# Optimization experiments

Measured on AMD Instinct MI355X. Metric: run time of the kernel, lower is better.

The kernel has to match this reference:

```python
import jax, jax.numpy as jnp
import numpy as np

NUM_HEADS = 16
EPS = 1e-8


def _dyn_quant(x):
    # per-token symmetric int8 quantization (dynamic input scale)
    s = jnp.maximum(jnp.max(jnp.abs(x), axis=-1, keepdims=True) / 127.0, EPS)
    q = jnp.clip(jnp.round(x / s), -127.0, 127.0)
    return q, s


def _quant_weight(w):
    # per-output-channel symmetric int8 weight quantization; w: [out, in]
    s = jnp.maximum(jnp.max(jnp.abs(w), axis=1, keepdims=True) / 127.0, EPS)
    q = jnp.clip(jnp.round(w / s), -127.0, 127.0)
    return q, s


def _w8a8_linear(x, w, b):
    # W8A8 GEMM with int32-exact accumulation (values fit exactly in fp32),
    # dequantized by per-token input scale * per-channel weight scale.
    qx, sx = _dyn_quant(x)          # [B,N,C], [B,N,1]
    qw, sw = _quant_weight(w)       # [O,C],   [O,1]
    y = jnp.einsum('bnc,oc->bno', qx, qw) * (sx * sw[:, 0])
    return y + b


def setup_inputs() -> dict:
    key = jax.random.key(0)
    ks = jax.random.split(key, 9)
    B, N, L, C = 2, 4096, 512, 2048
    sc = 0.02  # realistic weight init scale
    return {
        'x':    jax.random.normal(ks[0], (B, N, C), jnp.float32),
        'cond': jax.random.normal(ks[1], (B, L, C), jnp.float32),
        'mask': jnp.zeros((B, N, L), jnp.float32),  # additive attention mask
        'wq': jax.random.normal(ks[2], (C, C), jnp.float32) * sc,
        'bq': jnp.zeros((C,), jnp.float32),
        'wk': jax.random.normal(ks[3], (C, C), jnp.float32) * sc,
        'bk': jnp.zeros((C,), jnp.float32),
        'wv': jax.random.normal(ks[4], (C, C), jnp.float32) * sc,
        'bv': jnp.zeros((C,), jnp.float32),
        'wo': jax.random.normal(ks[5], (C, C), jnp.float32) * sc,
        'bo': jnp.zeros((C,), jnp.float32),
    }


def reference(x, cond, mask, wq, bq, wk, bk, wv, bv, wo, bo):
    B, N, C = x.shape
    L = cond.shape[1]
    H = NUM_HEADS
    D = C // H
    inv_sqrt_d = np.float32(1.0 / np.sqrt(D))

    # quantized Q projection, fp K/V projections
    q = _w8a8_linear(x, wq, bq).reshape(B, N, H, D).transpose(0, 2, 1, 3)      # [B,H,N,D]
    k = (cond @ wk.T + bk).reshape(B, L, H, D).transpose(0, 2, 1, 3)           # [B,H,L,D]
    v = (cond @ wv.T + bv).reshape(B, L, H, D).transpose(0, 2, 1, 3)           # [B,H,L,D]

    # SDPA cross-attention with additive mask broadcast over heads
    scores = jnp.einsum('bhnd,bhld->bhnl', q, k) * inv_sqrt_d + mask[:, None]
    attn = jax.nn.softmax(scores, axis=-1)
    o = jnp.einsum('bhnl,bhld->bhnd', attn, v)
    o = o.transpose(0, 2, 1, 3).reshape(B, N, C)

    # fused quant_sum (per-token requant) + quantized output projection
    return _w8a8_linear(o, wo, bo)
```

## Files before the change

kernel.cpp:

```cpp
#include <hip/hip_runtime.h>
#include <cstdint>
#include <cstddef>


typedef __bf16 bf16;
typedef __bf16 bf16x8 __attribute__((ext_vector_type(8)));
typedef __bf16 bf16x4 __attribute__((ext_vector_type(4)));
typedef float  f32x4  __attribute__((ext_vector_type(4)));
typedef int    i32x4  __attribute__((ext_vector_type(4)));

#define DEV __device__ __forceinline__

static constexpr int CB = 2;
static constexpr int CN = 4096;
static constexpr int CL = 512;
static constexpr int CC = 2048;
static constexpr int CH = 16;
static constexpr int CD = 128;
static constexpr int TOK = CB * CN;
static constexpr int LR  = CB * CL;

DEV void gl_lds16(const void* g, void* l) {
  __builtin_amdgcn_global_load_lds(
      (const __attribute__((address_space(1))) unsigned int*)g,
      (__attribute__((address_space(3))) unsigned int*)l, 16, 0, 0);
}

DEV f32x4 mfma16(bf16x8 a, bf16x8 b, f32x4 c) {
  return __builtin_amdgcn_mfma_f32_16x16x32_bf16(a, b, c, 0, 0, 0);
}

DEV i32x4 mfma_i8(i32x4 a, i32x4 b, i32x4 c) {
  return __builtin_amdgcn_mfma_i32_16x16x64_i8(a, b, c, 0, 0, 0);
}

__global__ __launch_bounds__(256) void quant_rows_i8(
    const float* __restrict__ in, signed char* __restrict__ q,
    float* __restrict__ scale)
{
  const int r = blockIdx.x, t = threadIdx.x;
  const float* x = in + (size_t)r * CC;
  const float4 v0 = ((const float4*)x)[2 * t];
  const float4 v1 = ((const float4*)x)[2 * t + 1];
  float m = fmaxf(fmaxf(fmaxf(fabsf(v0.x), fabsf(v0.y)), fmaxf(fabsf(v0.z), fabsf(v0.w))),
                  fmaxf(fmaxf(fabsf(v1.x), fabsf(v1.y)), fmaxf(fabsf(v1.z), fabsf(v1.w))));
#pragma unroll
  for (int off = 32; off > 0; off >>= 1) m = fmaxf(m, __shfl_xor(m, off));
  __shared__ float sm[4];
  if ((t & 63) == 0) sm[t >> 6] = m;
  __syncthreads();
  m = fmaxf(fmaxf(sm[0], sm[1]), fmaxf(sm[2], sm[3]));
  const float s = fmaxf(m / 127.0f, 1e-8f);
  if (t == 0) scale[r] = s;
  const float a[8] = {v0.x, v0.y, v0.z, v0.w, v1.x, v1.y, v1.z, v1.w};
  int2 pk;
  int lo = 0, hi = 0;
#pragma unroll
  for (int j = 0; j < 4; j++) {
    const int b0 = (int)fminf(fmaxf(rintf(a[j]     / s), -127.f), 127.f);
    const int b1 = (int)fminf(fmaxf(rintf(a[4 + j] / s), -127.f), 127.f);
    lo |= (b0 & 255) << (8 * j);
    hi |= (b1 & 255) << (8 * j);
  }
  pk.x = lo; pk.y = hi;
  const int c0 = t * 8;
  const int f = (r >> 1) & 3;
  const int pos = (c0 & ~63) | ((((c0 >> 4) & 3) ^ f) << 4) | (c0 & 15);
  *(int2*)&q[(size_t)r * CC + pos] = pk;
}

__global__ __launch_bounds__(256) void split_pair_k(
    const float* __restrict__ in, bf16* __restrict__ hi, bf16* __restrict__ lo)
{
  const size_t i = (size_t)blockIdx.x * 256 + threadIdx.x;
  const float4 v = ((const float4*)in)[i];
  const float a[4] = {v.x, v.y, v.z, v.w};
  bf16x4 h4, l4;
#pragma unroll
  for (int j = 0; j < 4; j++) {
    bf16 h = (bf16)a[j];
    h4[j] = h;
    l4[j] = (bf16)(a[j] - (float)h);
  }
  ((bf16x4*)hi)[i] = h4;
  ((bf16x4*)lo)[i] = l4;
}

__global__ __launch_bounds__(256) void bias_split_k(
    const float* __restrict__ in, const float* __restrict__ bias,
    bf16* __restrict__ hi, bf16* __restrict__ lo)
{
  const size_t i = (size_t)blockIdx.x * 256 + threadIdx.x;
  const float4 v = ((const float4*)in)[i];
  const float4 bb = ((const float4*)bias)[i & (CC / 4 - 1)];
  const float a[4] = {v.x + bb.x, v.y + bb.y, v.z + bb.z, v.w + bb.w};
  bf16x4 h4, l4;
#pragma unroll
  for (int j = 0; j < 4; j++) {
    bf16 h = (bf16)a[j];
    h4[j] = h;
    l4[j] = (bf16)(a[j] - (float)h);
  }
  ((bf16x4*)hi)[i] = h4;
  ((bf16x4*)lo)[i] = l4;
}

__global__ __launch_bounds__(256) void bias_split_vt_k(
    const float* __restrict__ Vf, const float* __restrict__ bias,
    bf16* __restrict__ vth, bf16* __restrict__ vtl)
{
  __shared__ float tile[32][33];
  const int t = threadIdx.x;
  const int l0 = blockIdx.x * 32, d0 = blockIdx.y * 32, bh = blockIdx.z;
  const int b = bh >> 4, h = bh & 15;
  const int r = t >> 3, c4 = (t & 7) * 4;
  const float4 v = *(const float4*)&Vf[((size_t)b * CL + l0 + r) * CC + h * CD + d0 + c4];
  const float4 bb = *(const float4*)&bias[h * CD + d0 + c4];
  tile[r][c4 + 0] = v.x + bb.x;
  tile[r][c4 + 1] = v.y + bb.y;
  tile[r][c4 + 2] = v.z + bb.z;
  tile[r][c4 + 3] = v.w + bb.w;
  __syncthreads();
  bf16x4 h4, l4;
#pragma unroll
  for (int j = 0; j < 4; j++) {
    const float a = tile[c4 + j][r];
    const bf16 hh = (bf16)a;
    h4[j] = hh;
    l4[j] = (bf16)(a - (float)hh);
  }
  const size_t o = ((size_t)bh * CD + d0 + r) * CL + l0 + c4;
  *(bf16x4*)&vth[o] = h4;
  *(bf16x4*)&vtl[o] = l4;
}

template <int MODE>
__global__ __launch_bounds__(256) void gemm_i8(
    const signed char* __restrict__ A, const signed char* __restrict__ B,
    float* __restrict__ out0, bf16* __restrict__ outH, bf16* __restrict__ outL,
    const float* __restrict__ rowS, const float* __restrict__ colS,
    const float* __restrict__ bias, const int Nd, const int K)
{
  __shared__ signed char sA[2][128 * 64] __attribute__((aligned(16)));
  __shared__ signed char sB[2][128 * 64] __attribute__((aligned(16)));
  const int t = threadIdx.x;
  const int m0 = blockIdx.y * 128, n0 = blockIdx.x * 128;
  const int srow = t >> 2, scol = (t & 3) * 16;
  const signed char* aP = A + (size_t)(m0 + srow) * K + scol;
  const signed char* bP = B + (size_t)(n0 + srow) * K + scol;
  const int lane = t & 63, wave = t >> 6;
  const int wm = (wave >> 1) * 64, wn = (wave & 1) * 64;
  const int quad = lane >> 4, l16 = lane & 15;
  i32x4 acc[4][4] = {};

  gl_lds16(aP,                  &sA[0][t * 16]);
  gl_lds16(aP + (size_t)64 * K, &sA[0][4096 + t * 16]);
  gl_lds16(bP,                  &sB[0][t * 16]);
  gl_lds16(bP + (size_t)64 * K, &sB[0][4096 + t * 16]);
  __syncthreads();

  int cur = 0;
  for (int kb = 0; kb < K; kb += 64) {
    const int nx = kb + 64;
    if (nx < K) {
      gl_lds16(aP + nx,                  &sA[cur ^ 1][t * 16]);
      gl_lds16(aP + nx + (size_t)64 * K, &sA[cur ^ 1][4096 + t * 16]);
      gl_lds16(bP + nx,                  &sB[cur ^ 1][t * 16]);
      gl_lds16(bP + nx + (size_t)64 * K, &sB[cur ^ 1][4096 + t * 16]);
    }
    i32x4 fa[4], fb[4];
#pragma unroll
    for (int i = 0; i < 4; i++) {
      const int ra = wm + i * 16 + l16;
      const int rb = wn + i * 16 + l16;
      fa[i] = *(const i32x4*)&sA[cur][ra * 64 + (quad ^ ((ra >> 1) & 3)) * 16];
      fb[i] = *(const i32x4*)&sB[cur][rb * 64 + (quad ^ ((rb >> 1) & 3)) * 16];
    }
#pragma unroll
    for (int mt = 0; mt < 4; mt++)
#pragma unroll
      for (int nt = 0; nt < 4; nt++)
        acc[mt][nt] = mfma_i8(fa[mt], fb[nt], acc[mt][nt]);
    __syncthreads();
    cur ^= 1;
  }

#pragma unroll
  for (int mt = 0; mt < 4; mt++)
#pragma unroll
    for (int nt = 0; nt < 4; nt++)
#pragma unroll
      for (int rg = 0; rg < 4; rg++) {
        const int mr = m0 + wm + mt * 16 + quad * 4 + rg;
        const int nc = n0 + wn + nt * 16 + l16;
        const float a = (float)acc[mt][nt][rg];
        const float sc = rowS[mr] * colS[nc];
        const float v = a * sc + bias[nc];
        if (MODE == 0) {
          out0[(size_t)mr * Nd + nc] = v;
        } else {
          const bf16 h = (bf16)v;
          outH[(size_t)mr * Nd + nc] = h;
          outL[(size_t)mr * Nd + nc] = (bf16)(v - (float)h);
        }
      }
}

__global__ __launch_bounds__(256) void gemm_kv(
    const bf16* __restrict__ Ah, const bf16* __restrict__ Al,
    const bf16* __restrict__ B0h, const bf16* __restrict__ B0l,
    const bf16* __restrict__ B1h, const bf16* __restrict__ B1l,
    float* __restrict__ out0, float* __restrict__ out1,
    const int Nd, const int K, const int kLen)
{
  __shared__ bf16 sAh[128 * 32] __attribute__((aligned(16)));
  __shared__ bf16 sBh[128 * 32] __attribute__((aligned(16)));
  __shared__ bf16 sAl[128 * 32] __attribute__((aligned(16)));
  __shared__ bf16 sBl[128 * 32] __attribute__((aligned(16)));
  const int t = threadIdx.x;
  const int kv = blockIdx.z >> 2, chunk = blockIdx.z & 3;
  const bf16* Bh = kv ? B1h : B0h;
  const bf16* Bl = kv ? B1l : B0l;
  float* outF = kv ? out1 : out0;
  const int m0 = blockIdx.y * 128, n0 = blockIdx.x * 128;
  const int k0 = chunk * kLen;
  const int srow = t >> 2, scol = (t & 3) * 8;
  const bf16* aP  = Ah + (size_t)(m0 + srow) * K + k0 + scol;
  const bf16* bP  = Bh + (size_t)(n0 + srow) * K + k0 + scol;
  const bf16* aPl = Al + (size_t)(m0 + srow) * K + k0 + scol;
  const bf16* bPl = Bl + (size_t)(n0 + srow) * K + k0 + scol;
  const int lane = t & 63, wave = t >> 6;
  const int wm = (wave >> 1) * 64, wn = (wave & 1) * 64;
  const int quad = lane >> 4, l16 = lane & 15;
  f32x4 acc[4][4] = {};

  for (int kb = 0; kb < kLen; kb += 32) {
    __syncthreads();
    gl_lds16(aP + kb,                   &sAh[t * 8]);
    gl_lds16(aP + kb + (size_t)64 * K,  &sAh[2048 + t * 8]);
    gl_lds16(bP + kb,                   &sBh[t * 8]);
    gl_lds16(bP + kb + (size_t)64 * K,  &sBh[2048 + t * 8]);
    gl_lds16(aPl + kb,                  &sAl[t * 8]);
    gl_lds16(aPl + kb + (size_t)64 * K, &sAl[2048 + t * 8]);
    gl_lds16(bPl + kb,                  &sBl[t * 8]);
    gl_lds16(bPl + kb + (size_t)64 * K, &sBl[2048 + t * 8]);
    __syncthreads();
    bf16x8 fa[4], fb[4], fal[4], fbl[4];
#pragma unroll
    for (int i = 0; i < 4; i++) {
      fa[i]  = *(const bf16x8*)&sAh[(wm + i * 16 + l16) * 32 + quad * 8];
      fb[i]  = *(const bf16x8*)&sBh[(wn + i * 16 + l16) * 32 + quad * 8];
      fal[i] = *(const bf16x8*)&sAl[(wm + i * 16 + l16) * 32 + quad * 8];
      fbl[i] = *(const bf16x8*)&sBl[(wn + i * 16 + l16) * 32 + quad * 8];
    }
#pragma unroll
    for (int mt = 0; mt < 4; mt++)
#pragma unroll
      for (int nt = 0; nt < 4; nt++) {
        f32x4 c = acc[mt][nt];
        c = mfma16(fa[mt],  fb[nt],  c);
        c = mfma16(fa[mt],  fbl[nt], c);
        c = mfma16(fal[mt], fb[nt],  c);
        acc[mt][nt] = c;
      }
  }

#pragma unroll
  for (int mt = 0; mt < 4; mt++)
#pragma unroll
    for (int nt = 0; nt < 4; nt++)
#pragma unroll
      for (int rg = 0; rg < 4; rg++) {
        const int mr = m0 + wm + mt * 16 + quad * 4 + rg;
        const int nc = n0 + wn + nt * 16 + l16;
        atomicAdd(&outF[(size_t)mr * Nd + nc], acc[mt][nt][rg]);
      }
}

__global__ __launch_bounds__(512) void attn_k(
    const bf16* __restrict__ qh, const bf16* __restrict__ ql,
    const bf16* __restrict__ kh, const bf16* __restrict__ kl,
    const bf16* __restrict__ vth, const bf16* __restrict__ vtl,
    const float* __restrict__ mask, float* __restrict__ O)
{
  __shared__ char arena[17408 + 20480 + 18432] __attribute__((aligned(16)));
  bf16 (*ks)[32][136] = (bf16 (*)[32][136])arena;
  bf16 (*vt)[128][40] = (bf16 (*)[128][40])(arena + 17408);
  float (*ps)[16][36] = (float (*)[16][36])(arena + 17408 + 20480);
  const int t = threadIdx.x, lane = t & 63, w = t >> 6;
  const int quad = lane >> 4, l16 = lane & 15;
  const int n0 = blockIdx.x * 128, h = blockIdx.y, b = blockIdx.z;
  const int bh = b * CH + h;
  const size_t qrow0 = (size_t)b * CN + n0;
  const float* mrow_base = mask + ((size_t)b * CN + n0 + w * 16 + quad * 4) * CL;

  const int krow = t >> 4, ksg = t & 15;
  const int vrow = t >> 2, vsg = t & 3;
  uint4 krh, krl, vrh, vrl;
  float mnx[2][4];
  {
    const size_t gro = ((size_t)b * CL + krow) * CC + h * CD + ksg * 8;
    krh = *(const uint4*)(kh + gro);
    krl = *(const uint4*)(kl + gro);
    const size_t gvo = ((size_t)bh * CD + vrow) * CL + vsg * 8;
    vrh = *(const uint4*)(vth + gvo);
    vrl = *(const uint4*)(vtl + gvo);
#pragma unroll
    for (int rg = 0; rg < 4; rg++) {
      const float* mrp = mrow_base + (size_t)rg * CL;
      mnx[0][rg] = mrp[l16];
      mnx[1][rg] = mrp[16 + l16];
    }
  }

  bf16x8 qfh[4], qfl[4];
  {
    bf16* qs = (bf16*)arena;
    const int row = t >> 2, sg = t & 3;
    {
      const bf16* src = qh + (qrow0 + row) * CC + h * CD + sg * 32;
      bf16* dst = qs + row * 136 + sg * 32;
#pragma unroll
      for (int j = 0; j < 4; j++) ((uint4*)dst)[j] = ((const uint4*)src)[j];
    }
    __syncthreads();
#pragma unroll
    for (int s = 0; s < 4; s++)
      qfh[s] = *(const bf16x8*)&qs[(w * 16 + l16) * 136 + s * 32 + quad * 8];
    __syncthreads();
    {
      const bf16* src = ql + (qrow0 + row) * CC + h * CD + sg * 32;
      bf16* dst = qs + row * 136 + sg * 32;
#pragma unroll
      for (int j = 0; j < 4; j++) ((uint4*)dst)[j] = ((const uint4*)src)[j];
    }
    __syncthreads();
#pragma unroll
    for (int s = 0; s < 4; s++)
      qfl[s] = *(const bf16x8*)&qs[(w * 16 + l16) * 136 + s * 32 + quad * 8];
  }

  f32x4 oacc[8] = {};
  f32x4 suma = {};
  const bf16 one = (bf16)1.0f;
  const bf16x8 ones = {one, one, one, one, one, one, one, one};
  const float isd = 0.08838834764831845f;

  for (int lc = 0; lc < CL; lc += 32) {
    __syncthreads();
    *(uint4*)&ks[0][krow][ksg * 8] = krh;
    *(uint4*)&ks[1][krow][ksg * 8] = krl;
    {
      const int vc = (vsg ^ ((vrow >> 3) & 3)) * 8;
      *(uint4*)&vt[0][vrow][vc] = vrh;
      *(uint4*)&vt[1][vrow][vc] = vrl;
    }
    float mcur[2][4];
#pragma unroll
    for (int rg = 0; rg < 4; rg++) {
      mcur[0][rg] = mnx[0][rg];
      mcur[1][rg] = mnx[1][rg];
    }
    __syncthreads();

    const int lcn = lc + 32;
    if (lcn < CL) {
      const size_t gro = ((size_t)b * CL + lcn + krow) * CC + h * CD + ksg * 8;
      krh = *(const uint4*)(kh + gro);
      krl = *(const uint4*)(kl + gro);
      const size_t gvo = ((size_t)bh * CD + vrow) * CL + lcn + vsg * 8;
      vrh = *(const uint4*)(vth + gvo);
      vrl = *(const uint4*)(vtl + gvo);
#pragma unroll
      for (int rg = 0; rg < 4; rg++) {
        const float* mrp = mrow_base + (size_t)rg * CL + lcn;
        mnx[0][rg] = mrp[l16];
        mnx[1][rg] = mrp[16 + l16];
      }
    }

    f32x4 sacc[2] = {};
    __builtin_amdgcn_s_setprio(1);
#pragma unroll
    for (int s = 0; s < 4; s++) {
#pragma unroll
      for (int lt = 0; lt < 2; lt++) {
        bf16x8 kbh = *(const bf16x8*)&ks[0][lt * 16 + l16][s * 32 + quad * 8];
        bf16x8 kbl = *(const bf16x8*)&ks[1][lt * 16 + l16][s * 32 + quad * 8];
        sacc[lt] = mfma16(qfh[s], kbh, sacc[lt]);
        sacc[lt] = mfma16(qfh[s], kbl, sacc[lt]);
        sacc[lt] = mfma16(qfl[s], kbh, sacc[lt]);
      }
    }
    __builtin_amdgcn_s_setprio(0);

    float u[2][4];
#pragma unroll
    for (int rg = 0; rg < 4; rg++) {
      u[0][rg] = __expf(sacc[0][rg] * isd + mcur[0][rg]);
      u[1][rg] = __expf(sacc[1][rg] * isd + mcur[1][rg]);
    }

#pragma unroll
    for (int lt = 0; lt < 2; lt++)
#pragma unroll
      for (int rg = 0; rg < 4; rg++)
        ps[w][quad * 4 + rg][lt * 16 + l16] = u[lt][rg];
    const float4 p0 = *(const float4*)&ps[w][l16][quad * 8];
    const float4 p1 = *(const float4*)&ps[w][l16][quad * 8 + 4];
    const float pv[8] = {p0.x, p0.y, p0.z, p0.w, p1.x, p1.y, p1.z, p1.w};
    bf16x8 ph, pl;
#pragma unroll
    for (int j = 0; j < 8; j++) {
      bf16 hh = (bf16)pv[j];
      ph[j] = hh;
      pl[j] = (bf16)(pv[j] - (float)hh);
    }

    suma = mfma16(ph, ones, suma);
    suma = mfma16(pl, ones, suma);
    __builtin_amdgcn_s_setprio(1);
#pragma unroll
    for (int nt = 0; nt < 8; nt++) {
      const int vr = nt * 16 + l16;
      const int vsw = (quad ^ ((vr >> 3) & 3)) * 8;
      bf16x8 vbh = *(const bf16x8*)&vt[0][vr][vsw];
      bf16x8 vbl = *(const bf16x8*)&vt[1][vr][vsw];
      f32x4 c = oacc[nt];
      c = mfma16(ph, vbh, c);
      c = mfma16(ph, vbl, c);
      c = mfma16(pl, vbh, c);
      oacc[nt] = c;
    }
    __builtin_amdgcn_s_setprio(0);
  }

  f32x4 inv;
#pragma unroll
  for (int rg = 0; rg < 4; rg++) inv[rg] = 1.0f / suma[rg];
#pragma unroll
  for (int nt = 0; nt < 8; nt++)
#pragma unroll
    for (int rg = 0; rg < 4; rg++) {
      const size_t row = qrow0 + w * 16 + quad * 4 + rg;
      O[row * CC + h * CD + nt * 16 + l16] = oacc[nt][rg] * inv[rg];
    }
}

extern "C" void kernel_launch(void* const* d_in, const int* in_sizes, int n_in,
                              void* d_out, int out_size, void* d_ws, size_t ws_size,
                              hipStream_t stream)
{
  (void)in_sizes; (void)n_in; (void)out_size; (void)ws_size;
  const float* x    = (const float*)d_in[0];
  const float* cond = (const float*)d_in[1];
  const float* mask = (const float*)d_in[2];
  const float* wq   = (const float*)d_in[3];
  const float* bq   = (const float*)d_in[4];
  const float* wk   = (const float*)d_in[5];
  const float* bk   = (const float*)d_in[6];
  const float* wv   = (const float*)d_in[7];
  const float* bv   = (const float*)d_in[8];
  const float* wo   = (const float*)d_in[9];
  const float* bo   = (const float*)d_in[10];
  float* out = (float*)d_out;

  char* wsb = (char*)d_ws;
  size_t off = 0;
  auto alloc = [&](size_t bytes) -> char* {
    char* p = wsb + off;
    off += (bytes + 255) & ~(size_t)255;
    return p;
  };
  signed char* qx  = (signed char*)alloc((size_t)TOK * CC);
  signed char* qwq = (signed char*)alloc((size_t)CC * CC);
  bf16* ch  = (bf16*)alloc((size_t)LR * CC * 2);
  bf16* cl_ = (bf16*)alloc((size_t)LR * CC * 2);
  bf16* wkh = (bf16*)alloc((size_t)CC * CC * 2);
  bf16* wkl = (bf16*)alloc((size_t)CC * CC * 2);
  bf16* wvh = (bf16*)alloc((size_t)CC * CC * 2);
  bf16* wvl = (bf16*)alloc((size_t)CC * CC * 2);
  float* Kf = (float*)alloc((size_t)LR * CC * 4);
  float* Vf = (float*)alloc((size_t)LR * CC * 4);
  float* Obuf = (float*)qx;
  bf16* qhb = (bf16*)alloc((size_t)TOK * CC * 2);
  bf16* qlb = (bf16*)alloc((size_t)TOK * CC * 2);
  bf16* khb = (bf16*)alloc((size_t)LR * CC * 2);
  bf16* klb = (bf16*)alloc((size_t)LR * CC * 2);
  bf16* vth = (bf16*)alloc((size_t)LR * CC * 2);
  bf16* vtl = (bf16*)alloc((size_t)LR * CC * 2);
  signed char* qwo = (signed char*)alloc((size_t)CC * CC);
  float* sx  = (float*)alloc((size_t)TOK * 4);
  float* swq = (float*)alloc((size_t)CC * 4);
  float* swo = (float*)alloc((size_t)CC * 4);
  float* sO  = (float*)alloc((size_t)TOK * 4);
  signed char* qO = (signed char*)qhb;

  quant_rows_i8<<<CC,  256, 0, stream>>>(wq, qwq, swq);
  quant_rows_i8<<<CC,  256, 0, stream>>>(wo, qwo, swo);
  quant_rows_i8<<<TOK, 256, 0, stream>>>(x, qx, sx);
  split_pair_k<<<(LR * CC / 4) / 256, 256, 0, stream>>>(cond, ch, cl_);
  split_pair_k<<<(CC * CC / 4) / 256, 256, 0, stream>>>(wk, wkh, wkl);
  split_pair_k<<<(CC * CC / 4) / 256, 256, 0, stream>>>(wv, wvh, wvl);
  gemm_i8<1><<<dim3(CC / 128, TOK / 128, 1), 256, 0, stream>>>(
      qx, qwq, nullptr, qhb, qlb, sx, swq, bq, CC, CC);
  (void)hipMemsetAsync(Kf, 0, (size_t)LR * CC * 4 * 2, stream);
  gemm_kv<<<dim3(CC / 128, LR / 128, 8), 256, 0, stream>>>(
      ch, cl_, wkh, wkl, wvh, wvl, Kf, Vf, CC, CC, 512);
  bias_split_k<<<(LR * CC / 4) / 256, 256, 0, stream>>>(Kf, bk, khb, klb);
  bias_split_vt_k<<<dim3(CL / 32, CD / 32, CB * CH), 256, 0, stream>>>(Vf, bv, vth, vtl);
  attn_k<<<dim3(CN / 128, CH, CB), 512, 0, stream>>>(
      qhb, qlb, khb, klb, vth, vtl, mask, Obuf);
  quant_rows_i8<<<TOK, 256, 0, stream>>>(Obuf, qO, sO);
  gemm_i8<0><<<dim3(CC / 128, TOK / 128, 1), 256, 0, stream>>>(
      qO, qwo, out, nullptr, nullptr, sO, swo, bo, CC, CC);
}
```

Before: 562.9 us.

## Swizzle block order for L2 locality and cut attention register pressure

Remaps the linear block index in the int8 GEMM, the KV GEMM and the attention kernel so that consecutive blocks are spread across strided tiles, aiming at better L2/XCD locality. In the attention kernel it adds a minimum-occupancy hint to launch bounds. It also drops the register-prefetched mask: the mask is now loaded directly for the current chunk, and the next V prefetch is moved after the score computation, which lowers live registers. The trade-off is that mask load latency is now exposed inside the loop and the V prefetch has less time to overlap with compute.

New measurement: 548.2 us. -2.6%, faster.

```diff
diff --git a/kernel.cpp b/kernel.cpp
--- a/kernel.cpp
+++ b/kernel.cpp
@@ -144,7 +144,9 @@
   __shared__ signed char sA[2][128 * 64] __attribute__((aligned(16)));
   __shared__ signed char sB[2][128 * 64] __attribute__((aligned(16)));
   const int t = threadIdx.x;
-  const int m0 = blockIdx.y * 128, n0 = blockIdx.x * 128;
+  int lin = blockIdx.y * 16 + blockIdx.x;
+  lin = (lin & 7) * 128 + (lin >> 3);
+  const int m0 = (lin >> 4) * 128, n0 = (lin & 15) * 128;
   const int srow = t >> 2, scol = (t & 3) * 16;
   const signed char* aP = A + (size_t)(m0 + srow) * K + scol;
   const signed char* bP = B + (size_t)(n0 + srow) * K + scol;
@@ -218,11 +220,14 @@
   __shared__ bf16 sAl[128 * 32] __attribute__((aligned(16)));
   __shared__ bf16 sBl[128 * 32] __attribute__((aligned(16)));
   const int t = threadIdx.x;
-  const int kv = blockIdx.z >> 2, chunk = blockIdx.z & 3;
+  int lin = (blockIdx.z * 8 + blockIdx.y) * 16 + blockIdx.x;
+  lin = (lin & 7) * 128 + (lin >> 3);
+  const int bx = lin & 15, by = (lin >> 4) & 7, bz = lin >> 7;
+  const int kv = bz >> 2, chunk = bz & 3;
   const bf16* Bh = kv ? B1h : B0h;
   const bf16* Bl = kv ? B1l : B0l;
   float* outF = kv ? out1 : out0;
-  const int m0 = blockIdx.y * 128, n0 = blockIdx.x * 128;
+  const int m0 = by * 128, n0 = bx * 128;
   const int k0 = chunk * kLen;
   const int srow = t >> 2, scol = (t & 3) * 8;
   const bf16* aP  = Ah + (size_t)(m0 + srow) * K + k0 + scol;
@@ -277,7 +282,7 @@
       }
 }
 
-__global__ __launch_bounds__(512) void attn_k(
+__global__ __launch_bounds__(512, 4) void attn_k(
     const bf16* __restrict__ qh, const bf16* __restrict__ ql,
     const bf16* __restrict__ kh, const bf16* __restrict__ kl,
     const bf16* __restrict__ vth, const bf16* __restrict__ vtl,
@@ -289,7 +294,11 @@
   float (*ps)[16][36] = (float (*)[16][36])(arena + 17408 + 20480);
   const int t = threadIdx.x, lane = t & 63, w = t >> 6;
   const int quad = lane >> 4, l16 = lane & 15;
-  const int n0 = blockIdx.x * 128, h = blockIdx.y, b = blockIdx.z;
+  int lin = (blockIdx.z * 16 + blockIdx.y) * 32 + blockIdx.x;
+  lin = (lin & 7) * 128 + (lin >> 3);
+  const int n0 = (lin & 31) * 128;
+  const int h  = (lin >> 5) & 15;
+  const int b  = lin >> 9;
   const int bh = b * CH + h;
   const size_t qrow0 = (size_t)b * CN + n0;
   const float* mrow_base = mask + ((size_t)b * CN + n0 + w * 16 + quad * 4) * CL;
@@ -297,7 +306,6 @@
   const int krow = t >> 4, ksg = t & 15;
   const int vrow = t >> 2, vsg = t & 3;
   uint4 krh, krl, vrh, vrl;
-  float mnx[2][4];
   {
     const size_t gro = ((size_t)b * CL + krow) * CC + h * CD + ksg * 8;
     krh = *(const uint4*)(kh + gro);
@@ -305,12 +313,6 @@
     const size_t gvo = ((size_t)bh * CD + vrow) * CL + vsg * 8;
     vrh = *(const uint4*)(vth + gvo);
     vrl = *(const uint4*)(vtl + gvo);
-#pragma unroll
-    for (int rg = 0; rg < 4; rg++) {
-      const float* mrp = mrow_base + (size_t)rg * CL;
-      mnx[0][rg] = mrp[l16];
-      mnx[1][rg] = mrp[16 + l16];
-    }
   }
 
   bf16x8 qfh[4], qfl[4];
@@ -355,28 +357,20 @@
       *(uint4*)&vt[0][vrow][vc] = vrh;
       *(uint4*)&vt[1][vrow][vc] = vrl;
     }
+    __syncthreads();
+
     float mcur[2][4];
 #pragma unroll
     for (int rg = 0; rg < 4; rg++) {
-      mcur[0][rg] = mnx[0][rg];
-      mcur[1][rg] = mnx[1][rg];
-    }
-    __syncthreads();
-
+      const float* mrp = mrow_base + (size_t)rg * CL + lc;
+      mcur[0][rg] = mrp[l16];
+      mcur[1][rg] = mrp[16 + l16];
+    }
     const int lcn = lc + 32;
     if (lcn < CL) {
       const size_t gro = ((size_t)b * CL + lcn + krow) * CC + h * CD + ksg * 8;
       krh = *(const uint4*)(kh + gro);
       krl = *(const uint4*)(kl + gro);
-      const size_t gvo = ((size_t)bh * CD + vrow) * CL + lcn + vsg * 8;
-      vrh = *(const uint4*)(vth + gvo);
-      vrl = *(const uint4*)(vtl + gvo);
-#pragma unroll
-      for (int rg = 0; rg < 4; rg++) {
-        const float* mrp = mrow_base + (size_t)rg * CL + lcn;
-        mnx[0][rg] = mrp[l16];
-        mnx[1][rg] = mrp[16 + l16];
-      }
     }
 
     f32x4 sacc[2] = {};
@@ -399,6 +393,12 @@
     for (int rg = 0; rg < 4; rg++) {
       u[0][rg] = __expf(sacc[0][rg] * isd + mcur[0][rg]);
       u[1][rg] = __expf(sacc[1][rg] * isd + mcur[1][rg]);
+    }
+
+    if (lcn < CL) {
+      const size_t gvo = ((size_t)bh * CD + vrow) * CL + lcn + vsg * 8;
+      vrh = *(const uint4*)(vth + gvo);
+      vrl = *(const uint4*)(vtl + gvo);
     }
 
 #pragma unroll
```
